# Kernel tuning notes

Measured on AMD Instinct MI355X. Metric: run time of the kernel, lower is better.

## Reference

```python
import jax, jax.numpy as jnp
import numpy as np

B, S, E, H = 4, 2048, 1024, 16
HD = E // H  # head_dim = 64


def setup_inputs() -> dict:
    key = jax.random.key(0)
    ks = jax.random.split(key, 9)
    s_in = 1.0 / np.sqrt(E)
    return {
        "x": jax.random.normal(ks[0], (B, S, E), dtype=jnp.float32),
        "Wq": jax.random.normal(ks[1], (E, E), dtype=jnp.float32) * s_in,
        "bq": jax.random.normal(ks[2], (E,), dtype=jnp.float32) * 0.01,
        "Wk": jax.random.normal(ks[3], (E, E), dtype=jnp.float32) * s_in,
        "bk": jax.random.normal(ks[4], (E,), dtype=jnp.float32) * 0.01,
        "Wv": jax.random.normal(ks[5], (E, E), dtype=jnp.float32) * s_in,
        "bv": jax.random.normal(ks[6], (E,), dtype=jnp.float32) * 0.01,
        "Wo": jax.random.normal(ks[7], (E, E), dtype=jnp.float32) * s_in,
        "bo": jax.random.normal(ks[8], (E,), dtype=jnp.float32) * 0.01,
    }


def reference(x, Wq, bq, Wk, bk, Wv, bv, Wo, bo):
    b, s, e = x.shape
    # fused QKV projections (equivalent to concatenated per-head linears)
    q = x @ Wq + bq  # [b, s, e]
    k = x @ Wk + bk
    v = x @ Wv + bv
    # split heads: [b, h, s, hd]
    def split(t):
        return t.reshape(b, s, H, HD).transpose(0, 2, 1, 3)
    q, k, v = split(q), split(k), split(v)
    scale = 1.0 / np.sqrt(HD)
    attn = jnp.einsum("bhqd,bhkd->bhqk", q, k) * scale  # [b, h, s, s]
    causal = jnp.tril(jnp.ones((s, s), dtype=bool))
    attn = jnp.where(causal[None, None], attn, -jnp.inf)
    attn = jax.nn.softmax(attn, axis=-1)
    y = jnp.einsum("bhqk,bhkd->bhqd", attn, v)  # [b, h, s, hd]
    y = y.transpose(0, 2, 1, 3).reshape(b, s, e)
    return y @ Wo + bo
```

## Files before the change

kernel.cpp:

```cpp
#include <hip/hip_runtime.h>
#include <hip/hip_bf16.h>

#define B_ 4
#define S_ 2048
#define E_ 1024
#define H_ 16
#define HD_ 64
#define QS 3072

typedef __attribute__((ext_vector_type(8))) short bf16x8;
typedef __attribute__((ext_vector_type(4))) float f32x4;

__device__ __forceinline__ float b2f(unsigned short u) {
    union { unsigned u; float f; } v; v.u = ((unsigned)u) << 16; return v.f;
}
__device__ __forceinline__ unsigned short f2b(float f) {
    union { float f; unsigned u; } v; v.f = f;
    unsigned lsb = (v.u >> 16) & 1u;
    v.u += 0x7fffu + lsb;
    return (unsigned short)(v.u >> 16);
}
__device__ __forceinline__ unsigned cvtpk_bf16(float lo, float hi) {
    unsigned r;
    asm("v_cvt_pk_bf16_f32 %0, %1, %2" : "=v"(r) : "v"(lo), "v"(hi));
    return r;
}

typedef const __attribute__((address_space(1))) unsigned glb_u32;
typedef __attribute__((address_space(3))) unsigned lds_u32;
__device__ __forceinline__ void gl_lds16(const unsigned short* g,
                                         unsigned short* l) {
    __builtin_amdgcn_global_load_lds((glb_u32*)g, (lds_u32*)l, 16, 0, 0);
}

__global__ void cvt_f32_to_bf16(const float* __restrict__ in,
                                unsigned short* __restrict__ out, int n8) {
    int i = blockIdx.x * blockDim.x + threadIdx.x;
    if (i >= n8) return;
    const float4* p = (const float4*)(in + (size_t)i * 8);
    float4 a = p[0], b = p[1];
    bf16x8 o;
    o[0] = (short)f2b(a.x); o[1] = (short)f2b(a.y);
    o[2] = (short)f2b(a.z); o[3] = (short)f2b(a.w);
    o[4] = (short)f2b(b.x); o[5] = (short)f2b(b.y);
    o[6] = (short)f2b(b.z); o[7] = (short)f2b(b.w);
    *(bf16x8*)(out + (size_t)i * 8) = o;
}

__global__ void transpose_cvt4(const float* __restrict__ W0,
                               const float* __restrict__ W1,
                               const float* __restrict__ W2,
                               const float* __restrict__ W3,
                               unsigned short* __restrict__ Wqkv,
                               unsigned short* __restrict__ Wto) {
    __shared__ float tile[32][33];
    int z = blockIdx.z;
    const float* W = (z == 0) ? W0 : (z == 1) ? W1 : (z == 2) ? W2 : W3;
    unsigned short* Wt = (z < 3) ? Wqkv + (size_t)z * 1024 * E_ : Wto;
    int tx = threadIdx.x, ty = threadIdx.y;
    int x0 = blockIdx.x * 32, y0 = blockIdx.y * 32;
#pragma unroll
    for (int j = 0; j < 32; j += 8)
        tile[ty + j][tx] = W[(size_t)(y0 + ty + j) * E_ + x0 + tx];
    __syncthreads();
#pragma unroll
    for (int j = 0; j < 32; j += 8)
        Wt[(size_t)(x0 + ty + j) * E_ + y0 + tx] = f2b(tile[tx][ty + j]);
}

#define BM 128
#define BN 128
#define BK 32

__global__ __launch_bounds__(256) void gemm_bt(
        const unsigned short* __restrict__ A,
        const unsigned short* __restrict__ Bt,
        const float* __restrict__ b0, const float* __restrict__ b1,
        const float* __restrict__ b2,
        unsigned short* __restrict__ Cb,
        int M, int N, int K) {
    __shared__ unsigned short As[BM][BK];
    __shared__ unsigned short Bs[BN][BK];
    int t = threadIdx.x;
    int lane = t & 63, wid = t >> 6;
    int wr = wid >> 1, wc = wid & 1;
    int nwg = gridDim.x * gridDim.y;
    int bid = blockIdx.y * gridDim.x + blockIdx.x;
    int ti = (bid & 7) * (nwg >> 3) + (bid >> 3);
    int bx = ti % gridDim.x, by = ti / gridDim.x;
    const int row = t >> 2, kc = (t & 3) << 3;
    const unsigned short* ga0 = A + (size_t)(by * BM + row) * K + kc;
    const unsigned short* gb0 = Bt + (size_t)(bx * BN + row) * K + kc;
    unsigned short* la0 = &As[0][0] + (size_t)t * 8;
    unsigned short* lb0 = &Bs[0][0] + (size_t)t * 8;
    const size_t step64 = (size_t)64 * K;

    f32x4 acc[4][4] = {};

    for (int ko = 0; ko < K; ko += BK) {
        gl_lds16(ga0 + ko, la0);
        gl_lds16(ga0 + ko + step64, la0 + 2048);
        gl_lds16(gb0 + ko, lb0);
        gl_lds16(gb0 + ko + step64, lb0 + 2048);
        __syncthreads();
        int kg = (lane >> 4) << 3;
        bf16x8 af[4], bfr[4];
#pragma unroll
        for (int i = 0; i < 4; ++i) {
            af[i]  = *(const bf16x8*)&As[wr * 64 + i * 16 + (lane & 15)][kg];
            bfr[i] = *(const bf16x8*)&Bs[wc * 64 + i * 16 + (lane & 15)][kg];
        }
#pragma unroll
        for (int i = 0; i < 4; ++i)
#pragma unroll
            for (int j = 0; j < 4; ++j)
                acc[i][j] = __builtin_amdgcn_mfma_f32_16x16x32_bf16(
                    af[i], bfr[j], acc[i][j], 0, 0, 0);
        __syncthreads();
    }

#pragma unroll
    for (int i = 0; i < 4; ++i) {
        int row0 = by * BM + wr * 64 + i * 16 + ((lane >> 4) << 2);
#pragma unroll
        for (int j = 0; j < 4; ++j) {
            int col = bx * BN + wc * 64 + j * 16 + (lane & 15);
            const float* bp = (col < 1024) ? b0 : ((col < 2048) ? b1 : b2);
            float bv = bp[col & 1023];
#pragma unroll
            for (int r = 0; r < 4; ++r) {
                int rr = row0 + r;
                Cb[(size_t)rr * N + col] = f2b(acc[i][j][r] + bv);
            }
        }
    }
}

__global__ __launch_bounds__(256) void gemm_bt_out(
        const unsigned short* __restrict__ A,
        const unsigned short* __restrict__ Bt,
        const float* __restrict__ bias,
        float* __restrict__ Cf, int M, int N, int K) {
    __shared__ unsigned short As[64][BK];
    __shared__ unsigned short Bs[BN][BK];
    int t = threadIdx.x;
    int lane = t & 63, wid = t >> 6;
    int wr = wid >> 1, wc = wid & 1;
    int nwg = gridDim.x * gridDim.y;
    int bid = blockIdx.y * gridDim.x + blockIdx.x;
    int ti = (bid & 7) * (nwg >> 3) + (bid >> 3);
    int bx = ti % gridDim.x, by = ti / gridDim.x;
    const int row = t >> 2, kc = (t & 3) << 3;
    const unsigned short* ga0 = A + (size_t)(by * 64 + row) * K + kc;
    const unsigned short* gb0 = Bt + (size_t)(bx * BN + row) * K + kc;
    unsigned short* la0 = &As[0][0] + (size_t)t * 8;
    unsigned short* lb0 = &Bs[0][0] + (size_t)t * 8;
    const size_t step64 = (size_t)64 * K;

    f32x4 acc[2][4] = {};

    for (int ko = 0; ko < K; ko += BK) {
        gl_lds16(ga0 + ko, la0);
        gl_lds16(gb0 + ko, lb0);
        gl_lds16(gb0 + ko + step64, lb0 + 2048);
        __syncthreads();
        int kg = (lane >> 4) << 3;
        bf16x8 af[2], bfr[4];
#pragma unroll
        for (int i = 0; i < 2; ++i)
            af[i] = *(const bf16x8*)&As[wr * 32 + i * 16 + (lane & 15)][kg];
#pragma unroll
        for (int j = 0; j < 4; ++j)
            bfr[j] = *(const bf16x8*)&Bs[wc * 64 + j * 16 + (lane & 15)][kg];
#pragma unroll
        for (int i = 0; i < 2; ++i)
#pragma unroll
            for (int j = 0; j < 4; ++j)
                acc[i][j] = __builtin_amdgcn_mfma_f32_16x16x32_bf16(
                    af[i], bfr[j], acc[i][j], 0, 0, 0);
        __syncthreads();
    }

#pragma unroll
    for (int i = 0; i < 2; ++i) {
        int row0 = by * 64 + wr * 32 + i * 16 + ((lane >> 4) << 2);
#pragma unroll
        for (int j = 0; j < 4; ++j) {
            int col = bx * BN + wc * 64 + j * 16 + (lane & 15);
            float bv = bias[col];
#pragma unroll
            for (int r = 0; r < 4; ++r)
                Cf[(size_t)(row0 + r) * N + col] = acc[i][j][r] + bv;
        }
    }
}

#define KVBLK 64

__global__ __launch_bounds__(512) void attn_mfma(
        const unsigned short* __restrict__ QKV,
        unsigned short* __restrict__ Yb) {
    __shared__ unsigned short Ks[2][KVBLK][64];
    __shared__ unsigned short Vt[2][64][KVBLK];
    __shared__ unsigned short Pl[8][16][64];

    int t = threadIdx.x;
    int lane = t & 63, wid = t >> 6;
    int l15 = lane & 15, lg = lane >> 4;
    int bh = blockIdx.x;
    int b = bh >> 4, h = bh & 15;
    int by = gridDim.y - 1 - blockIdx.y;
    int qbase = by * 256 + wid * 32;
    int vidx = lg << 4;

    const int kk = t >> 3;
    const int kg = ((t & 7) ^ (kk & 7)) << 3;
    const int vkey = t >> 3, vc = (t & 7) << 3;

    const unsigned short* kvbase = QKV + ((size_t)b * S_) * QS + 1024 + h * 64;

    const float qscale = 0.125f * 1.44269504f;
    bf16x8 qf[2][2];
#pragma unroll
    for (int mt = 0; mt < 2; ++mt)
#pragma unroll
        for (int ks = 0; ks < 2; ++ks) {
            int row = qbase + mt * 16 + l15;
            bf16x8 v = *(const bf16x8*)&QKV[((size_t)(b * S_ + row)) * QS +
                                            h * 64 + ks * 32 + lg * 8];
#pragma unroll
            for (int e = 0; e < 8; ++e)
                qf[mt][ks][e] = (short)f2b(b2f((unsigned short)v[e]) * qscale);
        }

    f32x4 yacc[2][4] = {};
    float m_[2] = {-1e30f, -1e30f}, l_[2] = {0.f, 0.f};

    int ntiles = by * 4 + 4;

    {
        gl_lds16(kvbase + (size_t)kk * QS + kg, &Ks[0][0][0] + (size_t)t * 8);
        const unsigned short* vsrc = kvbase + 1024 + (size_t)vkey * QS + vc;
        bf16x8 v0 = *(const bf16x8*)vsrc;
#pragma unroll
        for (int e = 0; e < 8; ++e) {
            int d = vc + e;
            int sig = e ^ (t & 7);
            Vt[0][d][vkey ^ (sig << 3)] = (unsigned short)v0[e];
        }
    }
    __syncthreads();

    int cur = 0;
    for (int kt = 0; kt < ntiles; ++kt) {
        int k0 = kt * KVBLK;
        bool pre = (kt + 1 < ntiles);
        bf16x8 nv0;
        if (pre) {
            const unsigned short* kb = kvbase + (size_t)(k0 + KVBLK) * QS;
            gl_lds16(kb + (size_t)kk * QS + kg,
                     &Ks[cur ^ 1][0][0] + (size_t)t * 8);
            nv0 = *(const bf16x8*)(kb + 1024 + (size_t)vkey * QS + vc);
        }

        if (k0 <= qbase + 31) {
            bool boundary = (k0 + KVBLK - 1 > qbase);
            f32x4 sacc[2][4] = {};
#pragma unroll
            for (int ks = 0; ks < 2; ++ks) {
                bf16x8 kf[4];
#pragma unroll
                for (int n = 0; n < 4; ++n)
                    kf[n] = *(const bf16x8*)&Ks[cur][n * 16 + l15]
                              [(ks * 32 + lg * 8) ^ ((l15 & 7) << 3)];
#pragma unroll
                for (int mt = 0; mt < 2; ++mt)
#pragma unroll
                    for (int n = 0; n < 4; ++n)
                        sacc[mt][n] = __builtin_amdgcn_mfma_f32_16x16x32_bf16(
                            kf[n], qf[mt][ks], sacc[mt][n], 0, 0, 0);
            }

#pragma unroll
            for (int mt = 0; mt < 2; ++mt) {
                int qv = qbase + mt * 16 + l15;
                if (boundary) {
#pragma unroll
                    for (int n = 0; n < 4; ++n)
#pragma unroll
                        for (int r = 0; r < 4; ++r)
                            if (k0 + n * 16 + lg * 4 + r > qv)
                                sacc[mt][n][r] = -3e38f;
                }
                float pm = -3e38f;
#pragma unroll
                for (int n = 0; n < 4; ++n)
#pragma unroll
                    for (int r = 0; r < 4; ++r)
                        pm = fmaxf(pm, sacc[mt][n][r]);
                pm = fmaxf(pm, __shfl_xor(pm, 16));
                pm = fmaxf(pm, __shfl_xor(pm, 32));
                float mo = m_[mt];
                float mn = mo;
                bool need = __any(pm > mo + 8.0f);
                if (need) {
                    mn = fmaxf(mo, pm);
                    float corr = __builtin_exp2f(mo - mn);
                    m_[mt] = mn;
                    l_[mt] *= corr;
                    int ci = __float_as_int(corr);
#pragma unroll
                    for (int r = 0; r < 4; ++r) {
                        float cq = __int_as_float(
                            __builtin_amdgcn_ds_bpermute(vidx + 4 * r, ci));
#pragma unroll
                        for (int n = 0; n < 4; ++n) yacc[mt][n][r] *= cq;
                    }
                }
                float rs = 0.f;
#pragma unroll
                for (int n = 0; n < 4; ++n)
#pragma unroll
                    for (int r = 0; r < 4; ++r) {
                        float p = __builtin_exp2f(sacc[mt][n][r] - mn);
                        sacc[mt][n][r] = p;
                        rs += p;
                    }
                rs += __shfl_xor(rs, 16);
                rs += __shfl_xor(rs, 32);
                l_[mt] += rs;
#pragma unroll
                for (int n = 0; n < 4; ++n)
#pragma unroll
                    for (int j = 0; j < 2; ++j) {
                        unsigned u = cvtpk_bf16(sacc[mt][n][2 * j],
                                                sacc[mt][n][2 * j + 1]);
                        int col = (n * 16 + lg * 4 + 2 * j) ^ ((l15 & 7) << 3);
                        *(unsigned*)&Pl[wid][l15][col] = u;
                    }
#pragma unroll
                for (int ks = 0; ks < 2; ++ks) {
                    bf16x8 pa, vf[4];
                    pa = *(const bf16x8*)&Pl[wid][l15]
                           [(ks * 32 + lg * 8) ^ ((l15 & 7) << 3)];
#pragma unroll
                    for (int nd = 0; nd < 4; ++nd) {
                        int d = nd * 16 + l15;
                        int sig = (d & 7) ^ ((d >> 3) & 7);
                        vf[nd] = *(const bf16x8*)&Vt[cur][d]
                                   [(ks * 32 + lg * 8) ^ (sig << 3)];
                    }
#pragma unroll
                    for (int nd = 0; nd < 4; ++nd)
                        yacc[mt][nd] = __builtin_amdgcn_mfma_f32_16x16x32_bf16(
                            pa, vf[nd], yacc[mt][nd], 0, 0, 0);
                }
            }
        }

        if (pre) {
#pragma unroll
            for (int e = 0; e < 8; ++e) {
                int d = vc + e;
                int sig = e ^ (t & 7);
                Vt[cur ^ 1][d][vkey ^ (sig << 3)] = (unsigned short)nv0[e];
            }
        }
        __syncthreads();
        cur ^= 1;
    }

#pragma unroll
    for (int mt = 0; mt < 2; ++mt) {
        float inv = 1.f / l_[mt];
        int ii = __float_as_int(inv);
        float iv[4];
#pragma unroll
        for (int r = 0; r < 4; ++r)
            iv[r] = __int_as_float(
                __builtin_amdgcn_ds_bpermute(vidx + 4 * r, ii));
#pragma unroll
        for (int n = 0; n < 4; ++n)
#pragma unroll
            for (int r = 0; r < 4; ++r) {
                int row = qbase + mt * 16 + lg * 4 + r;
                int d = n * 16 + l15;
                Yb[((size_t)(b * S_ + row)) * E_ + h * 64 + d] =
                    f2b(yacc[mt][n][r] * iv[r]);
            }
    }
}

extern "C" void kernel_launch(void* const* d_in, const int* in_sizes, int n_in,
                              void* d_out, int out_size, void* d_ws, size_t ws_size,
                              hipStream_t stream) {
    const float* x  = (const float*)d_in[0];
    const float* Wq = (const float*)d_in[1];
    const float* bq = (const float*)d_in[2];
    const float* Wk = (const float*)d_in[3];
    const float* bk = (const float*)d_in[4];
    const float* Wv = (const float*)d_in[5];
    const float* bv = (const float*)d_in[6];
    const float* Wo = (const float*)d_in[7];
    const float* bo = (const float*)d_in[8];

    char* ws = (char*)d_ws;
    const size_t M = (size_t)B_ * S_;
    unsigned short* xb   = (unsigned short*)ws;
    unsigned short* QKVb = (unsigned short*)(ws + (16ull << 20));
    unsigned short* Wqkv = (unsigned short*)(ws + (64ull << 20));
    unsigned short* Wto  = (unsigned short*)(ws + (70ull << 20));
    unsigned short* Yb   = xb;

    int n8 = (int)(M * E_ / 8);
    cvt_f32_to_bf16<<<(n8 + 255) / 256, 256, 0, stream>>>(x, xb, n8);

    dim3 tb(32, 8), tg(32, 32, 4);
    transpose_cvt4<<<tg, tb, 0, stream>>>(Wq, Wk, Wv, Wo, Wqkv, Wto);

    dim3 gq(QS / BN, M / BM);
    gemm_bt<<<gq, 256, 0, stream>>>(xb, Wqkv, bq, bk, bv, QKVb,
                                    (int)M, QS, E_);

    dim3 ag(B_ * H_, S_ / 256);
    attn_mfma<<<ag, 512, 0, stream>>>(QKVb, Yb);

    dim3 gg(E_ / BN, M / 64);
    gemm_bt_out<<<gg, 256, 0, stream>>>(Yb, Wto, bo, (float*)d_out,
                                        (int)M, E_, E_);
}
```

Baseline: 196.0 us.

## Double-buffer LDS tiles in QKV and output projection GEMMs

Both projection GEMM kernels now keep two LDS buffers for the A and B tiles. The first K-slice is loaded before the loop, and each iteration issues the load for the next slice into the other buffer before running MFMAs on the current one. This overlaps the global-to-LDS copy with matrix math and drops one barrier per K step. In exchange it doubles LDS use per block, which may lower occupancy, and the gain depends on the remaining barrier waiting for the async loads to finish.

```diff
diff --git a/kernel.cpp b/kernel.cpp
--- a/kernel.cpp
+++ b/kernel.cpp
@@ -79,8 +79,8 @@
         const float* __restrict__ b2,
         unsigned short* __restrict__ Cb,
         int M, int N, int K) {
-    __shared__ unsigned short As[BM][BK];
-    __shared__ unsigned short Bs[BN][BK];
+    __shared__ unsigned short As[2][BM][BK];
+    __shared__ unsigned short Bs[2][BN][BK];
     int t = threadIdx.x;
     int lane = t & 63, wid = t >> 6;
     int wr = wid >> 1, wc = wid & 1;
@@ -91,24 +91,34 @@
     const int row = t >> 2, kc = (t & 3) << 3;
     const unsigned short* ga0 = A + (size_t)(by * BM + row) * K + kc;
     const unsigned short* gb0 = Bt + (size_t)(bx * BN + row) * K + kc;
-    unsigned short* la0 = &As[0][0] + (size_t)t * 8;
-    unsigned short* lb0 = &Bs[0][0] + (size_t)t * 8;
+    unsigned short* la0 = &As[0][0][0] + (size_t)t * 8;
+    unsigned short* lb0 = &Bs[0][0][0] + (size_t)t * 8;
     const size_t step64 = (size_t)64 * K;
 
     f32x4 acc[4][4] = {};
 
+    gl_lds16(ga0, la0);
+    gl_lds16(ga0 + step64, la0 + 2048);
+    gl_lds16(gb0, lb0);
+    gl_lds16(gb0 + step64, lb0 + 2048);
+    __syncthreads();
+
+    int cur = 0;
     for (int ko = 0; ko < K; ko += BK) {
-        gl_lds16(ga0 + ko, la0);
-        gl_lds16(ga0 + ko + step64, la0 + 2048);
-        gl_lds16(gb0 + ko, lb0);
-        gl_lds16(gb0 + ko + step64, lb0 + 2048);
-        __syncthreads();
+        if (ko + BK < K) {
+            unsigned short* la = la0 + (cur ^ 1) * (BM * BK);
+            unsigned short* lb = lb0 + (cur ^ 1) * (BN * BK);
+            gl_lds16(ga0 + ko + BK, la);
+            gl_lds16(ga0 + ko + BK + step64, la + 2048);
+            gl_lds16(gb0 + ko + BK, lb);
+            gl_lds16(gb0 + ko + BK + step64, lb + 2048);
+        }
         int kg = (lane >> 4) << 3;
         bf16x8 af[4], bfr[4];
 #pragma unroll
         for (int i = 0; i < 4; ++i) {
-            af[i]  = *(const bf16x8*)&As[wr * 64 + i * 16 + (lane & 15)][kg];
-            bfr[i] = *(const bf16x8*)&Bs[wc * 64 + i * 16 + (lane & 15)][kg];
+            af[i]  = *(const bf16x8*)&As[cur][wr * 64 + i * 16 + (lane & 15)][kg];
+            bfr[i] = *(const bf16x8*)&Bs[cur][wc * 64 + i * 16 + (lane & 15)][kg];
         }
 #pragma unroll
         for (int i = 0; i < 4; ++i)
@@ -117,6 +127,7 @@
                 acc[i][j] = __builtin_amdgcn_mfma_f32_16x16x32_bf16(
                     af[i], bfr[j], acc[i][j], 0, 0, 0);
         __syncthreads();
+        cur ^= 1;
     }
 
 #pragma unroll
@@ -141,8 +152,8 @@
         const unsigned short* __restrict__ Bt,
         const float* __restrict__ bias,
         float* __restrict__ Cf, int M, int N, int K) {
-    __shared__ unsigned short As[64][BK];
-    __shared__ unsigned short Bs[BN][BK];
+    __shared__ unsigned short As[2][64][BK];
+    __shared__ unsigned short Bs[2][BN][BK];
     int t = threadIdx.x;
     int lane = t & 63, wid = t >> 6;
     int wr = wid >> 1, wc = wid & 1;
@@ -153,25 +164,34 @@
     const int row = t >> 2, kc = (t & 3) << 3;
     const unsigned short* ga0 = A + (size_t)(by * 64 + row) * K + kc;
     const unsigned short* gb0 = Bt + (size_t)(bx * BN + row) * K + kc;
-    unsigned short* la0 = &As[0][0] + (size_t)t * 8;
-    unsigned short* lb0 = &Bs[0][0] + (size_t)t * 8;
+    unsigned short* la0 = &As[0][0][0] + (size_t)t * 8;
+    unsigned short* lb0 = &Bs[0][0][0] + (size_t)t * 8;
     const size_t step64 = (size_t)64 * K;
 
     f32x4 acc[2][4] = {};
 
+    gl_lds16(ga0, la0);
+    gl_lds16(gb0, lb0);
+    gl_lds16(gb0 + step64, lb0 + 2048);
+    __syncthreads();
+
+    int cur = 0;
     for (int ko = 0; ko < K; ko += BK) {
-        gl_lds16(ga0 + ko, la0);
-        gl_lds16(gb0 + ko, lb0);
-        gl_lds16(gb0 + ko + step64, lb0 + 2048);
-        __syncthreads();
+        if (ko + BK < K) {
+            unsigned short* la = la0 + (cur ^ 1) * (64 * BK);
+            unsigned short* lb = lb0 + (cur ^ 1) * (BN * BK);
+            gl_lds16(ga0 + ko + BK, la);
+            gl_lds16(gb0 + ko + BK, lb);
+            gl_lds16(gb0 + ko + BK + step64, lb + 2048);
+        }
         int kg = (lane >> 4) << 3;
         bf16x8 af[2], bfr[4];
 #pragma unroll
         for (int i = 0; i < 2; ++i)
-            af[i] = *(const bf16x8*)&As[wr * 32 + i * 16 + (lane & 15)][kg];
+            af[i] = *(const bf16x8*)&As[cur][wr * 32 + i * 16 + (lane & 15)][kg];
 #pragma unroll
         for (int j = 0; j < 4; ++j)
-            bfr[j] = *(const bf16x8*)&Bs[wc * 64 + j * 16 + (lane & 15)][kg];
+            bfr[j] = *(const bf16x8*)&Bs[cur][wc * 64 + j * 16 + (lane & 15)][kg];
 #pragma unroll
         for (int i = 0; i < 2; ++i)
 #pragma unroll
@@ -179,6 +199,7 @@
                 acc[i][j] = __builtin_amdgcn_mfma_f32_16x16x32_bf16(
                     af[i], bfr[j], acc[i][j], 0, 0, 0);
         __syncthreads();
+        cur ^= 1;
     }
 
 #pragma unroll
```

After: 185.5 us, median of 2. 5.3% less time.
